# Performance work log

Measured on AMD Instinct MI355X. Metric: run time of the kernel, lower is better.

The kernel has to match this reference:

```python
import jax, jax.numpy as jnp
from jax import lax
import numpy as np

NEG = -1e9  # finite stand-in for -inf: keeps logaddexp grads NaN-free, exp underflows to 0
BLANK = 0
T_MAX, B, C = 256, 64, 8000
L_MAX = 32


def setup_inputs() -> dict:
    key = jax.random.key(0)
    k1, k2, k3, k4 = jax.random.split(key, 4)
    logits = jax.random.normal(k1, (T_MAX, B, C), dtype=jnp.float32)
    log_probs = jax.nn.log_softmax(logits, axis=-1)  # [T,B,C]
    targets = jax.random.randint(k2, (B, L_MAX), 1, C, dtype=jnp.int32)  # labels in [1,C), blank excluded
    input_lengths = jax.random.randint(k3, (B,), T_MAX // 2 + 1, T_MAX + 1, dtype=jnp.int32)
    target_lengths = jax.random.randint(k4, (B,), L_MAX // 2 + 1, L_MAX + 1, dtype=jnp.int32)
    return {"log_probs": log_probs, "targets": targets,
            "input_lengths": input_lengths, "target_lengths": target_lengths}


def _ctc_losses(log_probs, targets, input_lengths, target_lengths):
    T, Bb, Cc = log_probs.shape
    Lm = targets.shape[1]
    S = 2 * Lm + 1

    # extended targets: blank-interleaved labels, blank beyond 2L (matches torch buffer)
    lmask = jnp.arange(Lm)[None, :] < target_lengths[:, None]
    tgt = jnp.where(lmask, targets, BLANK)
    ext = jnp.full((Bb, S), BLANK, dtype=targets.dtype).at[:, 1::2].set(tgt)  # [B,S]

    ext_shift2 = jnp.concatenate(
        [jnp.full((Bb, 2), -1, dtype=ext.dtype), ext[:, :-2]], axis=1)
    skip = (ext != BLANK) & (ext != ext_shift2)  # [B,S]

    # emissions[t,b,s] = log_probs[t, b, ext[b,s]]
    emissions = jnp.take_along_axis(
        log_probs, jnp.broadcast_to(ext[None], (T, Bb, S)), axis=2)  # [T,B,S]

    # alpha init at t=0
    lp0 = log_probs[0]
    a0 = jnp.full((Bb, S), NEG, dtype=log_probs.dtype)
    a0 = a0.at[:, 0].set(lp0[:, BLANK])
    first_char = jnp.take_along_axis(lp0, ext[:, 1:2], axis=1)[:, 0]
    a0 = a0.at[:, 1].set(jnp.where(target_lengths > 0, first_char,
                                   jnp.full((Bb,), NEG, dtype=log_probs.dtype)))

    neg1 = jnp.full((Bb, 1), NEG, dtype=log_probs.dtype)
    neg2 = jnp.full((Bb, 2), NEG, dtype=log_probs.dtype)

    def step(alpha, em_t):
        p = jnp.logaddexp(alpha, jnp.concatenate([neg1, alpha[:, :-1]], axis=1))
        p = jnp.where(skip, jnp.logaddexp(p, jnp.concatenate([neg2, alpha[:, :-2]], axis=1)), p)
        new = p + em_t
        return new, new

    _, hist = lax.scan(step, a0, emissions[1:])
    alpha_hist = jnp.concatenate([a0[None], hist], axis=0)  # [T,B,S]

    final_alpha = alpha_hist[input_lengths - 1, jnp.arange(Bb)]  # [B,S]
    i_blank = 2 * target_lengths
    i_char = jnp.maximum(2 * target_lengths - 1, 0)
    v_blank = jnp.take_along_axis(final_alpha, i_blank[:, None], axis=1)[:, 0]
    v_char = jnp.take_along_axis(final_alpha, i_char[:, None], axis=1)[:, 0]
    total_log_prob = jnp.where(target_lengths > 0,
                               jnp.logaddexp(v_blank, v_char), v_blank)
    return -total_log_prob  # [B]


def reference(log_probs, targets, input_lengths, target_lengths):
    losses = _ctc_losses(log_probs, targets, input_lengths, target_lengths)
    safe_len = jnp.maximum(target_lengths, 1).astype(losses.dtype)
    return jnp.mean(losses / safe_len)  # reduction='mean'
```

## Files before the change

kernel.cpp:

```cpp
#include <hip/hip_runtime.h>
#include <cstdint>
#include <cstddef>


#define TMAX  256
#define BATCH 64
#define CNUM  8000
#define LMAX  32
#define SDIM  65
#define LOG2E 1.44269504088896340736f
#define LN2   0.69314718055994530942f
#define NEG2  (-1.0e9f * LOG2E)

__device__ __forceinline__ float hexp2(float x) { return __builtin_amdgcn_exp2f(x); }
__device__ __forceinline__ float hlog2(float x) { return __builtin_amdgcn_logf(x); }

__device__ __forceinline__ float lae3_log2(float a, float b, float c) {
    float m = fmaxf(fmaxf(a, b), c);
    float r = hexp2(a - m) + hexp2(b - m) + hexp2(c - m);
    return m + hlog2(r);
}

__global__ __launch_bounds__(64) void ctc_dp(
    const float* __restrict__ lp, const int* __restrict__ targets,
    const int* __restrict__ in_len, const int* __restrict__ tg_len,
    float* __restrict__ partial)
{
    const int b    = blockIdx.x;
    const int lane = threadIdx.x;
    const int Lb   = tg_len[b];
    const int Tb   = in_len[b];

    int  label = 0;
    bool skip  = false;
    if (lane & 1) {
        int k = lane >> 1;
        label = (k < Lb) ? targets[b * LMAX + k] : 0;
        int prev = (k >= 1) ? ((k - 1 < Lb) ? targets[b * LMAX + (k - 1)] : 0) : -1;
        skip = (label != 0) && (label != prev);
    }
    const bool use2 = skip && (lane >= 2);

    const float*  pbase   = lp + (size_t)b * CNUM + (size_t)label;
    const size_t  tstride = (size_t)BATCH * CNUM;

    float em0 = pbase[0];
    float a   = NEG2;
    if (lane == 0)            a = em0 * LOG2E;
    if (lane == 1 && Lb > 0)  a = em0 * LOG2E;
    float a64 = NEG2;

    const int steps  = Tb - 1;
    const int chunks = (steps + 15) >> 4;

    float ring[16];
    #pragma unroll
    for (int i = 0; i < 16; ++i) {
        int tl = 1 + i; if (tl > TMAX - 1) tl = TMAX - 1;
        ring[i] = pbase[(size_t)tl * tstride];
    }

    float a_res = a, a64_res = a64;
    int t = 1;
    for (int c = 0; c < chunks; ++c) {
        #pragma unroll
        for (int i = 0; i < 16; ++i, ++t) {
            float em2  = ring[i] * LOG2E;
            float em2b = __uint_as_float(
                __builtin_amdgcn_readfirstlane(__float_as_uint(em2)));

            float am1 = __shfl_up(a, 1, 64);
            float am2 = __shfl_up(a, 2, 64);
            am1 = (lane >= 1) ? am1 : NEG2;
            float am2p = use2 ? am2 : NEG2;

            float m64  = fmaxf(a64, a);
            float r64  = hexp2(a64 - m64) + hexp2(a - m64);
            float a64n = m64 + hlog2(r64) + em2b;

            a   = lae3_log2(a, am1, am2p) + em2;
            a64 = a64n;

            if (t == steps) { a_res = a; a64_res = a64; }

            int tl = t + 16; if (tl > TMAX - 1) tl = TMAX - 1;
            ring[i] = pbase[(size_t)tl * tstride];
        }
    }

    __shared__ float fin[SDIM];
    fin[lane] = a_res;
    if (lane == 63) fin[64] = a64_res;
    __syncthreads();

    if (lane == 0) {
        int iB = 2 * Lb;
        int iC = iB - 1; if (iC < 0) iC = 0;
        float vB = fin[iB];
        float vC = fin[iC];
        float tot2;
        if (Lb > 0) {
            float m = fmaxf(vB, vC);
            tot2 = m + hlog2(hexp2(vB - m) + hexp2(vC - m));
        } else {
            tot2 = vB;
        }
        float loss = -(tot2 * LN2);
        float sl   = (Lb > 0) ? (float)Lb : 1.0f;
        partial[b] = loss / sl;
    }
}

__global__ __launch_bounds__(64) void ctc_reduce(
    const float* __restrict__ partial, float* __restrict__ out)
{
    float v = partial[threadIdx.x];
    #pragma unroll
    for (int off = 32; off > 0; off >>= 1) v += __shfl_xor(v, off, 64);
    if (threadIdx.x == 0) out[0] = v * (1.0f / BATCH);
}

extern "C" void kernel_launch(void* const* d_in, const int* in_sizes, int n_in,
                              void* d_out, int out_size, void* d_ws, size_t ws_size,
                              hipStream_t stream) {
    const float* lp = (const float*)d_in[0];
    const int*   tg = (const int*)d_in[1];
    const int*   il = (const int*)d_in[2];
    const int*   tl = (const int*)d_in[3];
    float* partial  = (float*)d_ws;

    ctc_dp<<<dim3(BATCH), dim3(64), 0, stream>>>(lp, tg, il, tl, partial);
    ctc_reduce<<<dim3(1), dim3(64), 0, stream>>>(partial, (float*)d_out);
}
```

Measured before the change: 576.4 us.

## Prefetch all emissions into LDS with 256 threads before the serial DP

Each block now runs 256 threads that gather every timestep's blank and label log-probs into a shared-memory table in parallel. After that, one wavefront runs the serial alpha recursion reading emissions from LDS instead of issuing dependent global loads through a register ring. The final alpha values are fetched with lane shuffles rather than a shared buffer. Per-step global memory latency leaves the serial critical path, at the cost of an up-front gather phase (33 scattered loads per thread) and about 33KB of LDS per block.

```diff
diff --git a/kernel.cpp b/kernel.cpp
--- a/kernel.cpp
+++ b/kernel.cpp
@@ -21,15 +21,33 @@
     return m + hlog2(r);
 }
 
-__global__ __launch_bounds__(64) void ctc_dp(
+__global__ __launch_bounds__(256) void ctc_dp(
     const float* __restrict__ lp, const int* __restrict__ targets,
     const int* __restrict__ in_len, const int* __restrict__ tg_len,
     float* __restrict__ partial)
 {
-    const int b    = blockIdx.x;
-    const int lane = threadIdx.x;
-    const int Lb   = tg_len[b];
-    const int Tb   = in_len[b];
+    const int b   = blockIdx.x;
+    const int tid = threadIdx.x;
+    const int Lb  = tg_len[b];
+    const int Tb  = in_len[b];
+
+    __shared__ float s_em[TMAX][LMAX + 1];
+
+    {
+        const int t = tid;
+        const float* rowbase = lp + (size_t)t * (size_t)(BATCH * CNUM)
+                                  + (size_t)b * CNUM;
+        s_em[t][LMAX] = rowbase[0];
+        #pragma unroll
+        for (int k = 0; k < LMAX; ++k) {
+            int lab = (k < Lb) ? targets[b * LMAX + k] : 0;
+            s_em[t][k] = rowbase[lab];
+        }
+    }
+    __syncthreads();
+    if (tid >= 64) return;
+
+    const int lane = tid;
 
     int  label = 0;
     bool skip  = false;
@@ -41,63 +59,44 @@
     }
     const bool use2 = skip && (lane >= 2);
 
-    const float*  pbase   = lp + (size_t)b * CNUM + (size_t)label;
-    const size_t  tstride = (size_t)BATCH * CNUM;
+    const int col = (lane & 1) ? (lane >> 1) : LMAX;
 
-    float em0 = pbase[0];
+    float em0 = s_em[0][col];
     float a   = NEG2;
     if (lane == 0)            a = em0 * LOG2E;
     if (lane == 1 && Lb > 0)  a = em0 * LOG2E;
     float a64 = NEG2;
 
-    const int steps  = Tb - 1;
-    const int chunks = (steps + 15) >> 4;
+    const int steps = Tb - 1;
+    float emc = s_em[1][col];
+    for (int t = 1; t <= steps; ++t) {
+        int tn = (t < TMAX - 1) ? (t + 1) : (TMAX - 1);
+        float emn = s_em[tn][col];
 
-    float ring[16];
-    #pragma unroll
-    for (int i = 0; i < 16; ++i) {
-        int tl = 1 + i; if (tl > TMAX - 1) tl = TMAX - 1;
-        ring[i] = pbase[(size_t)tl * tstride];
+        float em2  = emc * LOG2E;
+        float em2b = __uint_as_float(
+            __builtin_amdgcn_readfirstlane(__float_as_uint(em2)));
+
+        float am1 = __shfl_up(a, 1, 64);
+        float am2 = __shfl_up(a, 2, 64);
+        am1 = (lane >= 1) ? am1 : NEG2;
+        float am2p = use2 ? am2 : NEG2;
+
+        float m64  = fmaxf(a64, a);
+        float r64  = hexp2(a64 - m64) + hexp2(a - m64);
+        float a64n = m64 + hlog2(r64) + em2b;
+
+        a   = lae3_log2(a, am1, am2p) + em2;
+        a64 = a64n;
+        emc = emn;
     }
 
-    float a_res = a, a64_res = a64;
-    int t = 1;
-    for (int c = 0; c < chunks; ++c) {
-        #pragma unroll
-        for (int i = 0; i < 16; ++i, ++t) {
-            float em2  = ring[i] * LOG2E;
-            float em2b = __uint_as_float(
-                __builtin_amdgcn_readfirstlane(__float_as_uint(em2)));
-
-            float am1 = __shfl_up(a, 1, 64);
-            float am2 = __shfl_up(a, 2, 64);
-            am1 = (lane >= 1) ? am1 : NEG2;
-            float am2p = use2 ? am2 : NEG2;
-
-            float m64  = fmaxf(a64, a);
-            float r64  = hexp2(a64 - m64) + hexp2(a - m64);
-            float a64n = m64 + hlog2(r64) + em2b;
-
-            a   = lae3_log2(a, am1, am2p) + em2;
-            a64 = a64n;
-
-            if (t == steps) { a_res = a; a64_res = a64; }
-
-            int tl = t + 16; if (tl > TMAX - 1) tl = TMAX - 1;
-            ring[i] = pbase[(size_t)tl * tstride];
-        }
-    }
-
-    __shared__ float fin[SDIM];
-    fin[lane] = a_res;
-    if (lane == 63) fin[64] = a64_res;
-    __syncthreads();
+    int iB = 2 * Lb;
+    int iC = iB - 1; if (iC < 0) iC = 0;
+    float vB = (iB < 64) ? __shfl(a, iB, 64) : __shfl(a64, 63, 64);
+    float vC = __shfl(a, iC, 64);
 
     if (lane == 0) {
-        int iB = 2 * Lb;
-        int iC = iB - 1; if (iC < 0) iC = 0;
-        float vB = fin[iB];
-        float vC = fin[iC];
         float tot2;
         if (Lb > 0) {
             float m = fmaxf(vB, vC);
@@ -129,6 +128,6 @@
     const int*   tl = (const int*)d_in[3];
     float* partial  = (float*)d_ws;
 
-    ctc_dp<<<dim3(BATCH), dim3(64), 0, stream>>>(lp, tg, il, tl, partial);
+    ctc_dp<<<dim3(BATCH), dim3(256), 0, stream>>>(lp, tg, il, tl, partial);
     ctc_reduce<<<dim3(1), dim3(64), 0, stream>>>(partial, (float*)d_out);
 }
```

After: 608.3 us. +5.5%, slower.
